# Kernel optimization log

Measured on AMD Instinct MI355X. Metric: run time of the kernel, lower is better.

## Reference

```python
import jax, jax.numpy as jnp
import numpy as np

B, H, S, D = 16, 12, 1024, 64  # batch, heads, seq, head_dim (dim=768, num_head=12)


def setup_inputs() -> dict:
    key = jax.random.key(0)
    ks = jax.random.split(key, 9)
    sc = 1.0 / np.sqrt(D)
    return {
        "x": jax.random.normal(ks[0], (B, H, S, D), dtype=jnp.float32),
        "Wq": jax.random.normal(ks[1], (D, D), dtype=jnp.float32) * sc,
        "bq": jax.random.normal(ks[2], (D,), dtype=jnp.float32) * 0.02,
        "Wk": jax.random.normal(ks[3], (D, D), dtype=jnp.float32) * sc,
        "bk": jax.random.normal(ks[4], (D,), dtype=jnp.float32) * 0.02,
        "Wv": jax.random.normal(ks[5], (D, D), dtype=jnp.float32) * sc,
        "bv": jax.random.normal(ks[6], (D,), dtype=jnp.float32) * 0.02,
        "Wo": jax.random.normal(ks[7], (D, D), dtype=jnp.float32) * sc,
        "bo": jax.random.normal(ks[8], (D,), dtype=jnp.float32) * 0.02,
    }


def reference(x, Wq, bq, Wk, bk, Wv, bv, Wo, bo):
    # torch Linear: y = x @ W^T + b, applied to last dim (head_dim)
    q = jnp.einsum("bhsd,ed->bhse", x, Wq) + bq
    k = jnp.einsum("bhsd,ed->bhse", x, Wk) + bk
    v = jnp.einsum("bhsd,ed->bhse", x, Wv) + bv
    scores = jnp.einsum("bhqd,bhkd->bhqk", q, k) / jnp.sqrt(jnp.float32(q.shape[-1]))
    attn = jax.nn.softmax(scores, axis=-1)
    out = jnp.einsum("bhqk,bhkd->bhqd", attn, v)
    out = jnp.einsum("bhsd,ed->bhse", out, Wo) + bo
    return out
```

## Files before the change

kernel.cpp:

```cpp
#include <hip/hip_runtime.h>
#include <math.h>


typedef __bf16 bf16x8 __attribute__((ext_vector_type(8)));
typedef float  f32x4  __attribute__((ext_vector_type(4)));

#define MFMA(a, b, c) __builtin_amdgcn_mfma_f32_16x16x32_bf16((a), (b), (c), 0, 0, 0)

static constexpr int S = 1024;
static constexpr int PAD = 72;
static constexpr size_t NE = 196608ull * 64ull;
static constexpr float QSCALE = 0.125f * 1.4426950408889634f;

__device__ inline unsigned long long pack4bf(float a, float b, float c, float d) {
    union { __bf16 h[4]; unsigned long long u; } pk;
    pk.h[0] = (__bf16)a; pk.h[1] = (__bf16)b; pk.h[2] = (__bf16)c; pk.h[3] = (__bf16)d;
    return pk.u;
}

union frag_u { bf16x8 v; unsigned long long u[2]; };

__global__ void wo_conv(const float* __restrict__ Wo, __bf16* __restrict__ wob) {
    int p = (blockIdx.x * 256 + threadIdx.x) * 4;
    int e = p >> 6, s = p & 63;
    int h = s >> 5, qp = (s >> 3) & 3, tb = (s >> 2) & 1;
    int d0 = 32 * h + 16 * tb + 4 * qp;
    float4 v = *(const float4*)(Wo + e * 64 + d0);
    *(unsigned long long*)(wob + p) = pack4bf(v.x, v.y, v.z, v.w);
}

__global__ __launch_bounds__(256) void proj_qkv(
    const float* __restrict__ x,
    const float* __restrict__ Wq, const float* __restrict__ bq,
    const float* __restrict__ Wk, const float* __restrict__ bk,
    const float* __restrict__ Wv, const float* __restrict__ bv,
    __bf16* __restrict__ gq, __bf16* __restrict__ gk, __bf16* __restrict__ gvt)
{
    __shared__ __align__(16) __bf16 lx[128][PAD];
    __shared__ __align__(16) __bf16 lw[3][64][PAD];
    __shared__ __align__(16) __bf16 lbuf[128][PAD];
    __shared__ float lb[3][64];

    const int tid = threadIdx.x;
    const int row_base = blockIdx.x * 128;

    #pragma unroll
    for (int i = tid * 4; i < 8192; i += 1024) {
        float4 v = *(const float4*)(x + (size_t)row_base * 64 + i);
        int r = i >> 6, c = i & 63;
        *(unsigned long long*)&lx[r][c] = pack4bf(v.x, v.y, v.z, v.w);
    }
    const float* Ws[3] = {Wq, Wk, Wv};
    #pragma unroll
    for (int mtx = 0; mtx < 3; mtx++) {
        #pragma unroll
        for (int i = tid * 4; i < 4096; i += 1024) {
            float4 v = *(const float4*)(Ws[mtx] + i);
            int r = i >> 6, c = i & 63;
            *(unsigned long long*)&lw[mtx][r][c] = pack4bf(v.x, v.y, v.z, v.w);
        }
    }
    if (tid < 64) { lb[0][tid] = bq[tid]; lb[1][tid] = bk[tid]; lb[2][tid] = bv[tid]; }
    __syncthreads();

    const int w = tid >> 6, lane = tid & 63, m = lane & 15, quad = lane >> 4;
    const int bh = row_base >> 10;
    const int s_base = row_base & 1023;

    bf16x8 xf[2][2];
    #pragma unroll
    for (int g = 0; g < 2; g++) {
        xf[g][0] = *(const bf16x8*)&lx[w * 32 + g * 16 + m][quad * 8];
        xf[g][1] = *(const bf16x8*)&lx[w * 32 + g * 16 + m][32 + quad * 8];
    }

    #pragma unroll
    for (int mtx = 0; mtx < 2; mtx++) {
        #pragma unroll
        for (int et = 0; et < 4; et++) {
            bf16x8 wf0 = *(const bf16x8*)&lw[mtx][et * 16 + m][quad * 8];
            bf16x8 wf1 = *(const bf16x8*)&lw[mtx][et * 16 + m][32 + quad * 8];
            float4 bias = *(const float4*)&lb[mtx][et * 16 + quad * 4];
            #pragma unroll
            for (int g = 0; g < 2; g++) {
                f32x4 acc = {0.f, 0.f, 0.f, 0.f};
                acc = MFMA(wf0, xf[g][0], acc);
                acc = MFMA(wf1, xf[g][1], acc);
                unsigned long long u;
                if (mtx == 0)
                    u = pack4bf((acc[0] + bias.x) * QSCALE, (acc[1] + bias.y) * QSCALE,
                                (acc[2] + bias.z) * QSCALE, (acc[3] + bias.w) * QSCALE);
                else
                    u = pack4bf(acc[0] + bias.x, acc[1] + bias.y,
                                acc[2] + bias.z, acc[3] + bias.w);
                *(unsigned long long*)&lbuf[w * 32 + g * 16 + m][et * 16 + quad * 4] = u;
            }
        }
        __syncthreads();
        __bf16* dst = (mtx == 0 ? gq : gk);
        #pragma unroll
        for (int it = 0; it < 4; it++) {
            int idx = it * 256 + tid;
            int row = idx >> 3, col = (idx & 7) * 8;
            *(uint4*)(dst + ((size_t)row_base + row) * 64 + col) = *(uint4*)&lbuf[row][col];
        }
        __syncthreads();
    }

    __bf16 (*lvt)[136] = (__bf16(*)[136])&lbuf[0][0];
    #pragma unroll
    for (int et = 0; et < 4; et++) {
        bf16x8 wf0 = *(const bf16x8*)&lw[2][et * 16 + m][quad * 8];
        bf16x8 wf1 = *(const bf16x8*)&lw[2][et * 16 + m][32 + quad * 8];
        const float bias = lb[2][et * 16 + m];
        #pragma unroll
        for (int g = 0; g < 2; g++) {
            f32x4 acc = {0.f, 0.f, 0.f, 0.f};
            acc = MFMA(xf[g][0], wf0, acc);
            acc = MFMA(xf[g][1], wf1, acc);
            const int tp = (2 * w + g) & 3;
            const int p0 = 64 * (w >> 1) + 32 * (tp >> 1) + 8 * quad + 4 * (tp & 1);
            *(unsigned long long*)&lvt[et * 16 + m][p0] =
                pack4bf(acc[0] + bias, acc[1] + bias, acc[2] + bias, acc[3] + bias);
        }
    }
    __syncthreads();
    #pragma unroll
    for (int it = 0; it < 4; it++) {
        int idx = it * 256 + tid;
        int row = idx >> 4, col = (idx & 15) * 8;
        *(uint4*)(gvt + ((size_t)bh * 64 + row) * 1024 + s_base + col) = *(uint4*)&lvt[row][col];
    }
}

__global__ __launch_bounds__(256) void attn(
    const __bf16* __restrict__ gq, const __bf16* __restrict__ gk,
    const __bf16* __restrict__ gvt, const __bf16* __restrict__ wob,
    const float* __restrict__ bo, float* __restrict__ out)
{
    __shared__ __align__(16) __bf16 lk[64][PAD];
    __shared__ __align__(16) __bf16 lv[64][PAD];

    const int tid = threadIdx.x;
    const int w = tid >> 6, lane = tid & 63, m = lane & 15, quad = lane >> 4;
    const int bh = blockIdx.x;
    const int q0 = blockIdx.y * 256 + w * 64;

    bf16x8 qf[4][2];
    #pragma unroll
    for (int g = 0; g < 4; g++) {
        const __bf16* qrow = gq + ((size_t)bh * S + q0 + g * 16 + m) * 64;
        qf[g][0] = *(const bf16x8*)(qrow + quad * 8);
        qf[g][1] = *(const bf16x8*)(qrow + 32 + quad * 8);
    }

    f32x4 o[4][4];
    float lsum[4] = {0.f, 0.f, 0.f, 0.f};
    #pragma unroll
    for (int g = 0; g < 4; g++)
        #pragma unroll
        for (int n = 0; n < 4; n++) o[g][n] = {0.f, 0.f, 0.f, 0.f};

    const int sr = tid >> 3;
    const int sc = (tid & 7) * 8;
    const __bf16* kbase = gk + (size_t)bh * S * 64;
    const __bf16* vbase = gvt + (size_t)bh * 64 * 1024;

    uint4 kreg0 = *(const uint4*)(kbase + (size_t)sr * 64 + sc);
    uint4 kreg1 = *(const uint4*)(kbase + (size_t)(sr + 32) * 64 + sc);
    uint4 vreg0 = *(const uint4*)(vbase + (size_t)sr * 1024 + sc);
    uint4 vreg1 = *(const uint4*)(vbase + (size_t)(sr + 32) * 1024 + sc);

    for (int kb = 0; kb < 16; kb++) {
        __syncthreads();
        *(uint4*)&lk[sr][sc]      = kreg0;
        *(uint4*)&lk[sr + 32][sc] = kreg1;
        *(uint4*)&lv[sr][sc]      = vreg0;
        *(uint4*)&lv[sr + 32][sc] = vreg1;
        if (kb < 15) {
            const int nb = (kb + 1) * 64;
            kreg0 = *(const uint4*)(kbase + (size_t)(nb + sr) * 64 + sc);
            kreg1 = *(const uint4*)(kbase + (size_t)(nb + sr + 32) * 64 + sc);
            vreg0 = *(const uint4*)(vbase + (size_t)sr * 1024 + nb + sc);
            vreg1 = *(const uint4*)(vbase + (size_t)(sr + 32) * 1024 + nb + sc);
        }
        __syncthreads();

        #pragma unroll
        for (int gp = 0; gp < 2; gp++) {
            frag_u pb[2][2];
            #pragma unroll
            for (int t = 0; t < 4; t++) {
                bf16x8 ka0 = *(const bf16x8*)&lk[t * 16 + m][quad * 8];
                bf16x8 ka1 = *(const bf16x8*)&lk[t * 16 + m][32 + quad * 8];
                #pragma unroll
                for (int gl = 0; gl < 2; gl++) {
                    const int g = gp * 2 + gl;
                    f32x4 acc = {0.f, 0.f, 0.f, 0.f};
                    acc = MFMA(ka0, qf[g][0], acc);
                    acc = MFMA(ka1, qf[g][1], acc);
                    float e0 = __builtin_amdgcn_exp2f(acc[0]);
                    float e1 = __builtin_amdgcn_exp2f(acc[1]);
                    float e2 = __builtin_amdgcn_exp2f(acc[2]);
                    float e3 = __builtin_amdgcn_exp2f(acc[3]);
                    lsum[g] += (e0 + e1) + (e2 + e3);
                    pb[gl][t >> 1].u[t & 1] = pack4bf(e0, e1, e2, e3);
                }
            }
            #pragma unroll
            for (int n = 0; n < 4; n++) {
                bf16x8 va0 = *(const bf16x8*)&lv[n * 16 + m][quad * 8];
                bf16x8 va1 = *(const bf16x8*)&lv[n * 16 + m][32 + quad * 8];
                #pragma unroll
                for (int gl = 0; gl < 2; gl++) {
                    const int g = gp * 2 + gl;
                    o[g][n] = MFMA(va0, pb[gl][0].v, o[g][n]);
                    o[g][n] = MFMA(va1, pb[gl][1].v, o[g][n]);
                }
            }
        }
    }

    #pragma unroll
    for (int g = 0; g < 4; g++) {
        lsum[g] += __shfl_xor(lsum[g], 16);
        lsum[g] += __shfl_xor(lsum[g], 32);
    }

    bf16x8 wf[4][2];
    #pragma unroll
    for (int et = 0; et < 4; et++) {
        wf[et][0] = *(const bf16x8*)(wob + (size_t)(et * 16 + m) * 64 + quad * 8);
        wf[et][1] = *(const bf16x8*)(wob + (size_t)(et * 16 + m) * 64 + 32 + quad * 8);
    }
    float biasr[4];
    #pragma unroll
    for (int et = 0; et < 4; et++) biasr[et] = bo[et * 16 + m];

    #pragma unroll
    for (int g = 0; g < 4; g++) {
        const float inv = 1.f / lsum[g];
        frag_u af0, af1;
        af0.u[0] = pack4bf(o[g][0][0] * inv, o[g][0][1] * inv, o[g][0][2] * inv, o[g][0][3] * inv);
        af0.u[1] = pack4bf(o[g][1][0] * inv, o[g][1][1] * inv, o[g][1][2] * inv, o[g][1][3] * inv);
        af1.u[0] = pack4bf(o[g][2][0] * inv, o[g][2][1] * inv, o[g][2][2] * inv, o[g][2][3] * inv);
        af1.u[1] = pack4bf(o[g][3][0] * inv, o[g][3][1] * inv, o[g][3][2] * inv, o[g][3][3] * inv);
        #pragma unroll
        for (int et = 0; et < 4; et++) {
            f32x4 acc = {0.f, 0.f, 0.f, 0.f};
            acc = MFMA(af0.v, wf[et][0], acc);
            acc = MFMA(af1.v, wf[et][1], acc);
            #pragma unroll
            for (int r = 0; r < 4; r++) {
                size_t row = (size_t)bh * S + q0 + g * 16 + quad * 4 + r;
                out[row * 64 + et * 16 + m] = acc[r] + biasr[et];
            }
        }
    }
}

extern "C" void kernel_launch(void* const* d_in, const int* in_sizes, int n_in,
                              void* d_out, int out_size, void* d_ws, size_t ws_size,
                              hipStream_t stream) {
    const float* x  = (const float*)d_in[0];
    const float* Wq = (const float*)d_in[1];
    const float* bq = (const float*)d_in[2];
    const float* Wk = (const float*)d_in[3];
    const float* bk = (const float*)d_in[4];
    const float* Wv = (const float*)d_in[5];
    const float* bv = (const float*)d_in[6];
    const float* Wo = (const float*)d_in[7];
    const float* bo = (const float*)d_in[8];
    float* out = (float*)d_out;

    __bf16* gq  = (__bf16*)d_ws;
    __bf16* gk  = gq + NE;
    __bf16* gvt = gk + NE;
    __bf16* wob = gvt + NE;

    wo_conv<<<4, 256, 0, stream>>>(Wo, wob);
    proj_qkv<<<1536, 256, 0, stream>>>(x, Wq, bq, Wk, bk, Wv, bv, gq, gk, gvt);
    attn<<<dim3(192, 4), 256, 0, stream>>>(gq, gk, gvt, wob, bo, out);
}
```

Measured before the change: 196.7 us.

## Drop Wo conversion kernel, pre-swizzle weights in LDS, simplify K/V staging

```diff
diff --git a/kernel.cpp b/kernel.cpp
--- a/kernel.cpp
+++ b/kernel.cpp
@@ -20,16 +20,7 @@
 
 union frag_u { bf16x8 v; unsigned long long u[2]; };
 
-__global__ void wo_conv(const float* __restrict__ Wo, __bf16* __restrict__ wob) {
-    int p = (blockIdx.x * 256 + threadIdx.x) * 4;
-    int e = p >> 6, s = p & 63;
-    int h = s >> 5, qp = (s >> 3) & 3, tb = (s >> 2) & 1;
-    int d0 = 32 * h + 16 * tb + 4 * qp;
-    float4 v = *(const float4*)(Wo + e * 64 + d0);
-    *(unsigned long long*)(wob + p) = pack4bf(v.x, v.y, v.z, v.w);
-}
-
-__global__ __launch_bounds__(256) void proj_qkv(
+__global__ __launch_bounds__(256, 3) void proj(
     const float* __restrict__ x,
     const float* __restrict__ Wq, const float* __restrict__ bq,
     const float* __restrict__ Wk, const float* __restrict__ bk,
@@ -37,8 +28,8 @@
     __bf16* __restrict__ gq, __bf16* __restrict__ gk, __bf16* __restrict__ gvt)
 {
     __shared__ __align__(16) __bf16 lx[128][PAD];
-    __shared__ __align__(16) __bf16 lw[3][64][PAD];
     __shared__ __align__(16) __bf16 lbuf[128][PAD];
+    __shared__ __align__(16) __bf16 lw[3][8][64][8];
     __shared__ float lb[3][64];
 
     const int tid = threadIdx.x;
@@ -50,15 +41,18 @@
         int r = i >> 6, c = i & 63;
         *(unsigned long long*)&lx[r][c] = pack4bf(v.x, v.y, v.z, v.w);
     }
-    const float* Ws[3] = {Wq, Wk, Wv};
-    #pragma unroll
-    for (int mtx = 0; mtx < 3; mtx++) {
-        #pragma unroll
-        for (int i = tid * 4; i < 4096; i += 1024) {
-            float4 v = *(const float4*)(Ws[mtx] + i);
-            int r = i >> 6, c = i & 63;
-            *(unsigned long long*)&lw[mtx][r][c] = pack4bf(v.x, v.y, v.z, v.w);
-        }
+    #pragma unroll
+    for (int c = tid; c < 1536; c += 256) {
+        int mtx = c >> 9, rest = c & 511;
+        int fe = rest >> 6, ln = rest & 63;
+        int mm = ln & 15, qq = ln >> 4;
+        int et = fe >> 1, half = fe & 1;
+        const float* src = (mtx == 0 ? Wq : mtx == 1 ? Wk : Wv)
+                           + (size_t)(et * 16 + mm) * 64 + half * 32 + qq * 8;
+        float4 u0 = *(const float4*)(src);
+        float4 u1 = *(const float4*)(src + 4);
+        *(unsigned long long*)&lw[mtx][fe][ln][0] = pack4bf(u0.x, u0.y, u0.z, u0.w);
+        *(unsigned long long*)&lw[mtx][fe][ln][4] = pack4bf(u1.x, u1.y, u1.z, u1.w);
     }
     if (tid < 64) { lb[0][tid] = bq[tid]; lb[1][tid] = bk[tid]; lb[2][tid] = bv[tid]; }
     __syncthreads();
@@ -78,8 +72,8 @@
     for (int mtx = 0; mtx < 2; mtx++) {
         #pragma unroll
         for (int et = 0; et < 4; et++) {
-            bf16x8 wf0 = *(const bf16x8*)&lw[mtx][et * 16 + m][quad * 8];
-            bf16x8 wf1 = *(const bf16x8*)&lw[mtx][et * 16 + m][32 + quad * 8];
+            bf16x8 wf0 = *(const bf16x8*)&lw[mtx][et * 2 + 0][lane][0];
+            bf16x8 wf1 = *(const bf16x8*)&lw[mtx][et * 2 + 1][lane][0];
             float4 bias = *(const float4*)&lb[mtx][et * 16 + quad * 4];
             #pragma unroll
             for (int g = 0; g < 2; g++) {
@@ -110,8 +104,8 @@
     __bf16 (*lvt)[136] = (__bf16(*)[136])&lbuf[0][0];
     #pragma unroll
     for (int et = 0; et < 4; et++) {
-        bf16x8 wf0 = *(const bf16x8*)&lw[2][et * 16 + m][quad * 8];
-        bf16x8 wf1 = *(const bf16x8*)&lw[2][et * 16 + m][32 + quad * 8];
+        bf16x8 wf0 = *(const bf16x8*)&lw[2][et * 2 + 0][lane][0];
+        bf16x8 wf1 = *(const bf16x8*)&lw[2][et * 2 + 1][lane][0];
         const float bias = lb[2][et * 16 + m];
         #pragma unroll
         for (int g = 0; g < 2; g++) {
@@ -133,9 +127,9 @@
     }
 }
 
-__global__ __launch_bounds__(256) void attn(
+__global__ __launch_bounds__(256, 3) void attn(
     const __bf16* __restrict__ gq, const __bf16* __restrict__ gk,
-    const __bf16* __restrict__ gvt, const __bf16* __restrict__ wob,
+    const __bf16* __restrict__ gvt, const float* __restrict__ Wo,
     const float* __restrict__ bo, float* __restrict__ out)
 {
     __shared__ __align__(16) __bf16 lk[64][PAD];
@@ -166,26 +160,22 @@
     const __bf16* kbase = gk + (size_t)bh * S * 64;
     const __bf16* vbase = gvt + (size_t)bh * 64 * 1024;
 
-    uint4 kreg0 = *(const uint4*)(kbase + (size_t)sr * 64 + sc);
-    uint4 kreg1 = *(const uint4*)(kbase + (size_t)(sr + 32) * 64 + sc);
-    uint4 vreg0 = *(const uint4*)(vbase + (size_t)sr * 1024 + sc);
-    uint4 vreg1 = *(const uint4*)(vbase + (size_t)(sr + 32) * 1024 + sc);
-
     for (int kb = 0; kb < 16; kb++) {
         __syncthreads();
-        *(uint4*)&lk[sr][sc]      = kreg0;
-        *(uint4*)&lk[sr + 32][sc] = kreg1;
-        *(uint4*)&lv[sr][sc]      = vreg0;
-        *(uint4*)&lv[sr + 32][sc] = vreg1;
-        if (kb < 15) {
-            const int nb = (kb + 1) * 64;
-            kreg0 = *(const uint4*)(kbase + (size_t)(nb + sr) * 64 + sc);
-            kreg1 = *(const uint4*)(kbase + (size_t)(nb + sr + 32) * 64 + sc);
-            vreg0 = *(const uint4*)(vbase + (size_t)sr * 1024 + nb + sc);
-            vreg1 = *(const uint4*)(vbase + (size_t)(sr + 32) * 1024 + nb + sc);
-        }
-        __syncthreads();
-
+        {
+            const int nb = kb * 64;
+            uint4 k0 = *(const uint4*)(kbase + (size_t)(nb + sr) * 64 + sc);
+            uint4 k1 = *(const uint4*)(kbase + (size_t)(nb + sr + 32) * 64 + sc);
+            uint4 v0 = *(const uint4*)(vbase + (size_t)sr * 1024 + nb + sc);
+            uint4 v1 = *(const uint4*)(vbase + (size_t)(sr + 32) * 1024 + nb + sc);
+            *(uint4*)&lk[sr][sc]      = k0;
+            *(uint4*)&lk[sr + 32][sc] = k1;
+            *(uint4*)&lv[sr][sc]      = v0;
+            *(uint4*)&lv[sr + 32][sc] = v1;
+        }
+        __syncthreads();
+
+        __builtin_amdgcn_s_setprio(1);
         #pragma unroll
         for (int gp = 0; gp < 2; gp++) {
             frag_u pb[2][2];
@@ -219,6 +209,7 @@
                 }
             }
         }
+        __builtin_amdgcn_s_setprio(0);
     }
 
     #pragma unroll
@@ -230,8 +221,18 @@
     bf16x8 wf[4][2];
     #pragma unroll
     for (int et = 0; et < 4; et++) {
-        wf[et][0] = *(const bf16x8*)(wob + (size_t)(et * 16 + m) * 64 + quad * 8);
-        wf[et][1] = *(const bf16x8*)(wob + (size_t)(et * 16 + m) * 64 + 32 + quad * 8);
+        const float* worow = Wo + (size_t)(et * 16 + m) * 64;
+        float4 c0 = *(const float4*)(worow + 4 * quad);
+        float4 c1 = *(const float4*)(worow + 16 + 4 * quad);
+        float4 c2 = *(const float4*)(worow + 32 + 4 * quad);
+        float4 c3 = *(const float4*)(worow + 48 + 4 * quad);
+        frag_u f0, f1;
+        f0.u[0] = pack4bf(c0.x, c0.y, c0.z, c0.w);
+        f0.u[1] = pack4bf(c1.x, c1.y, c1.z, c1.w);
+        f1.u[0] = pack4bf(c2.x, c2.y, c2.z, c2.w);
+        f1.u[1] = pack4bf(c3.x, c3.y, c3.z, c3.w);
+        wf[et][0] = f0.v;
+        wf[et][1] = f1.v;
     }
     float biasr[4];
     #pragma unroll
@@ -276,9 +277,7 @@
     __bf16* gq  = (__bf16*)d_ws;
     __bf16* gk  = gq + NE;
     __bf16* gvt = gk + NE;
-    __bf16* wob = gvt + NE;
-
-    wo_conv<<<4, 256, 0, stream>>>(Wo, wob);
-    proj_qkv<<<1536, 256, 0, stream>>>(x, Wq, bq, Wk, bk, Wv, bv, gq, gk, gvt);
-    attn<<<dim3(192, 4), 256, 0, stream>>>(gq, gk, gvt, wob, bo, out);
-}
+
+    proj<<<1536, 256, 0, stream>>>(x, Wq, bq, Wk, bk, Wv, bv, gq, gk, gvt);
+    attn<<<dim3(192, 4), 256, 0, stream>>>(gq, gk, gvt, Wo, bo, out);
+}
```

Result: slower. 231.5 us (+17.7%).
